# Optimization experiments

Measured on AMD Instinct MI355X. Metric: run time of the kernel, lower is better.

The kernel has to match this reference:

```python
import jax, jax.numpy as jnp
import numpy as np

NUM_QUERIES = 300


def setup_inputs() -> dict:
    key = jax.random.key(0)
    k1, k2, k3 = jax.random.split(key, 3)
    d_model = 256
    tokens = jax.random.normal(k1, (16, 20000, d_model), dtype=jnp.float32)
    # nn.Linear(d_model, 1): weight [1, d_model], bias [1]; store as vector/scalar
    W = jax.random.normal(k2, (d_model,), dtype=jnp.float32) / np.sqrt(d_model)
    b = jax.random.normal(k3, (), dtype=jnp.float32) * 0.01
    return {"tokens": tokens, "W": W, "b": b}


def reference(tokens, W, b):
    # scores: [B, N] -- scalar linear projection per token
    scores = jnp.einsum("bnd,d->bn", tokens, W) + b
    k = min(NUM_QUERIES, tokens.shape[1])
    _, topk = jax.lax.top_k(scores, k)  # [B, k], sorted by descending score
    # gather full token vectors at selected indices: [B, k, d]
    selected = jnp.take_along_axis(tokens, topk[..., None], axis=1)
    return selected, topk
```

## Files before the change

### kernel.cpp

```cpp
#include <hip/hip_runtime.h>
#include <stdint.h>

#define B 16
#define N 20000
#define D 256
#define K 300

__global__ __launch_bounds__(256) void score_kernel(
    const float* __restrict__ tokens, const float* __restrict__ W,
    const float* __restrict__ bias, uint32_t* __restrict__ keys) {
  int gwave = (blockIdx.x * blockDim.x + threadIdx.x) >> 6;
  int lane = threadIdx.x & 63;
  if (gwave >= B * N) return;
  const float4 w4 = ((const float4*)W)[lane];
  const float4 t4 = ((const float4*)(tokens + (size_t)gwave * D))[lane];
  float dot = t4.x * w4.x + t4.y * w4.y + t4.z * w4.z + t4.w * w4.w;
#pragma unroll
  for (int off = 32; off >= 1; off >>= 1) dot += __shfl_xor(dot, off, 64);
  if (lane == 0) {
    float s = dot + bias[0];
    uint32_t u = __float_as_uint(s);
    keys[gwave] = (u & 0x80000000u) ? ~u : (u | 0x80000000u);
  }
}

__global__ __launch_bounds__(1024) void topk_kernel(
    const uint32_t* __restrict__ keys_g, int* __restrict__ idx_out,
    float* __restrict__ out_idx_f) {
  __shared__ uint32_t hist[256];
  __shared__ uint32_t s_prefix, s_remaining, cand_cnt;
  __shared__ uint64_t cand[512];

  const int b = blockIdx.x;
  const int t = threadIdx.x;
  const uint32_t* keys = keys_g + (size_t)b * N;

  if (t == 0) {
    s_prefix = 0;
    s_remaining = K;
    cand_cnt = 0;
  }
  __syncthreads();

  for (int pass = 0; pass < 4; ++pass) {
    int shift = 24 - pass * 8;
    if (t < 256) hist[t] = 0;
    __syncthreads();
    uint32_t prefix = s_prefix;
    uint32_t pmask = (pass == 0) ? 0u : (0xFFFFFFFFu << (shift + 8));
    for (int i = t; i < N; i += 1024) {
      uint32_t k = keys[i];
      if ((k & pmask) == prefix) atomicAdd(&hist[(k >> shift) & 0xFFu], 1u);
    }
    __syncthreads();
    if (t == 0) {
      uint32_t rem = s_remaining;
      uint32_t acc = 0;
      int bin = 255;
      for (; bin > 0; --bin) {
        if (acc + hist[bin] >= rem) break;
        acc += hist[bin];
      }
      s_prefix = prefix | ((uint32_t)bin << shift);
      s_remaining = rem - acc;
    }
    __syncthreads();
  }
  const uint32_t T = s_prefix;

  for (int i = t; i < N; i += 1024) {
    uint32_t k = keys[i];
    if (k >= T) {
      uint32_t pos = atomicAdd(&cand_cnt, 1u);
      if (pos < 512)
        cand[pos] = ((uint64_t)k << 32) | (uint64_t)(0xFFFFFFFFu - (uint32_t)i);
    }
  }
  __syncthreads();
  int cnt = (int)cand_cnt;
  if (cnt > 512) cnt = 512;
  if (t < 512 && t >= cnt) cand[t] = 0;
  __syncthreads();

  for (int ksz = 2; ksz <= 512; ksz <<= 1) {
    for (int j = ksz >> 1; j >= 1; j >>= 1) {
      if (t < 512) {
        int ixj = t ^ j;
        if (ixj > t) {
          uint64_t a = cand[t], c = cand[ixj];
          bool desc = ((t & ksz) == 0);
          if (desc ? (a < c) : (a > c)) {
            cand[t] = c;
            cand[ixj] = a;
          }
        }
      }
      __syncthreads();
    }
  }

  if (t < K) {
    int idx = (int)(0xFFFFFFFFu - (uint32_t)(cand[t] & 0xFFFFFFFFu));
    idx_out[b * K + t] = idx;
    out_idx_f[b * K + t] = (float)idx;
  }
}

__global__ __launch_bounds__(256) void gather_kernel(
    const float* __restrict__ tokens, const int* __restrict__ idx,
    float* __restrict__ out0) {
  int gwave = (blockIdx.x * blockDim.x + threadIdx.x) >> 6;
  int lane = threadIdx.x & 63;
  if (gwave >= B * K) return;
  int b = gwave / K;
  int id = idx[gwave];
  float4 v = ((const float4*)(tokens + ((size_t)b * N + id) * D))[lane];
  ((float4*)(out0 + (size_t)gwave * D))[lane] = v;
}

extern "C" void kernel_launch(void* const* d_in, const int* in_sizes, int n_in,
                              void* d_out, int out_size, void* d_ws,
                              size_t ws_size, hipStream_t stream) {
  const float* tokens = (const float*)d_in[0];
  const float* W = (const float*)d_in[1];
  const float* bias = (const float*)d_in[2];

  float* out_sel = (float*)d_out;
  float* out_idx_f = out_sel + (size_t)B * K * D;

  uint32_t* keys = (uint32_t*)d_ws;
  int* idx = (int*)((char*)d_ws + (size_t)B * N * sizeof(uint32_t));

  score_kernel<<<(B * N + 3) / 4, 256, 0, stream>>>(tokens, W, bias, keys);
  topk_kernel<<<B, 1024, 0, stream>>>(keys, idx, out_idx_f);
  gather_kernel<<<(B * K + 3) / 4, 256, 0, stream>>>(tokens, idx, out_sel);
}
```

Before: 479.4 us.

## Score four tokens per wave and parallelize top-k histogram scan

The score kernel now has each wave process four consecutive tokens, issuing four independent float4 loads and interleaved shuffle reductions, and storing the four keys with a single uint4 write. The top-k kernel reads keys as uint4, and replaces the serial single-thread bin scan with a 64-lane wave prefix scan to pick the threshold bin. It also clears the histogram at the end of each pass, which removes one barrier per pass. The goal is more memory-level parallelism in the bandwidth-bound scoring pass and less serial latency in the radix select, at the cost of more registers and a launch grid that assumes B*N is divisible by 16.

```diff
diff --git a/kernel.cpp b/kernel.cpp
--- a/kernel.cpp
+++ b/kernel.cpp
@@ -9,72 +9,119 @@
 __global__ __launch_bounds__(256) void score_kernel(
     const float* __restrict__ tokens, const float* __restrict__ W,
     const float* __restrict__ bias, uint32_t* __restrict__ keys) {
-  int gwave = (blockIdx.x * blockDim.x + threadIdx.x) >> 6;
+  int wid = (blockIdx.x * blockDim.x + threadIdx.x) >> 6;
   int lane = threadIdx.x & 63;
-  if (gwave >= B * N) return;
+  int tb = wid * 4;
+  if (tb >= B * N) return;
   const float4 w4 = ((const float4*)W)[lane];
-  const float4 t4 = ((const float4*)(tokens + (size_t)gwave * D))[lane];
-  float dot = t4.x * w4.x + t4.y * w4.y + t4.z * w4.z + t4.w * w4.w;
+  const float4* tp = (const float4*)(tokens + (size_t)tb * D);
+  float4 a0 = tp[lane];
+  float4 a1 = tp[64 + lane];
+  float4 a2 = tp[128 + lane];
+  float4 a3 = tp[192 + lane];
+  float d0 = a0.x * w4.x + a0.y * w4.y + a0.z * w4.z + a0.w * w4.w;
+  float d1 = a1.x * w4.x + a1.y * w4.y + a1.z * w4.z + a1.w * w4.w;
+  float d2 = a2.x * w4.x + a2.y * w4.y + a2.z * w4.z + a2.w * w4.w;
+  float d3 = a3.x * w4.x + a3.y * w4.y + a3.z * w4.z + a3.w * w4.w;
 #pragma unroll
-  for (int off = 32; off >= 1; off >>= 1) dot += __shfl_xor(dot, off, 64);
+  for (int off = 32; off >= 1; off >>= 1) {
+    d0 += __shfl_xor(d0, off, 64);
+    d1 += __shfl_xor(d1, off, 64);
+    d2 += __shfl_xor(d2, off, 64);
+    d3 += __shfl_xor(d3, off, 64);
+  }
   if (lane == 0) {
-    float s = dot + bias[0];
-    uint32_t u = __float_as_uint(s);
-    keys[gwave] = (u & 0x80000000u) ? ~u : (u | 0x80000000u);
+    float bb = bias[0];
+    float s0 = d0 + bb, s1 = d1 + bb, s2 = d2 + bb, s3 = d3 + bb;
+    uint32_t u0 = __float_as_uint(s0), u1 = __float_as_uint(s1);
+    uint32_t u2 = __float_as_uint(s2), u3 = __float_as_uint(s3);
+    uint4 kv;
+    kv.x = (u0 & 0x80000000u) ? ~u0 : (u0 | 0x80000000u);
+    kv.y = (u1 & 0x80000000u) ? ~u1 : (u1 | 0x80000000u);
+    kv.z = (u2 & 0x80000000u) ? ~u2 : (u2 | 0x80000000u);
+    kv.w = (u3 & 0x80000000u) ? ~u3 : (u3 | 0x80000000u);
+    ((uint4*)keys)[wid] = kv;
   }
 }
 
 __global__ __launch_bounds__(1024) void topk_kernel(
     const uint32_t* __restrict__ keys_g, int* __restrict__ idx_out,
     float* __restrict__ out_idx_f) {
-  __shared__ uint32_t hist[256];
-  __shared__ uint32_t s_prefix, s_remaining, cand_cnt;
+  __shared__ __align__(16) uint32_t hist[256];
   __shared__ uint64_t cand[512];
+  __shared__ uint32_t s_prefix, s_remaining, s_prefix_next, s_rem_next,
+      cand_cnt;
 
   const int b = blockIdx.x;
   const int t = threadIdx.x;
-  const uint32_t* keys = keys_g + (size_t)b * N;
+  const uint4* keys4 = (const uint4*)(keys_g + (size_t)b * N);
+  const int N4 = N / 4;
 
   if (t == 0) {
     s_prefix = 0;
     s_remaining = K;
     cand_cnt = 0;
   }
+  if (t < 256) hist[t] = 0;
   __syncthreads();
 
   for (int pass = 0; pass < 4; ++pass) {
-    int shift = 24 - pass * 8;
-    if (t < 256) hist[t] = 0;
+    const int shift = 24 - pass * 8;
+    const uint32_t prefix = s_prefix;
+    const uint32_t pmask = (pass == 0) ? 0u : (0xFFFFFFFFu << (shift + 8));
+    for (int i = t; i < N4; i += 1024) {
+      uint4 kv = keys4[i];
+      uint32_t ka[4] = {kv.x, kv.y, kv.z, kv.w};
+#pragma unroll
+      for (int j = 0; j < 4; ++j)
+        if ((ka[j] & pmask) == prefix)
+          atomicAdd(&hist[(ka[j] >> shift) & 255u], 1u);
+    }
     __syncthreads();
-    uint32_t prefix = s_prefix;
-    uint32_t pmask = (pass == 0) ? 0u : (0xFFFFFFFFu << (shift + 8));
-    for (int i = t; i < N; i += 1024) {
-      uint32_t k = keys[i];
-      if ((k & pmask) == prefix) atomicAdd(&hist[(k >> shift) & 0xFFu], 1u);
+    if (t < 64) {
+      uint4 h = ((const uint4*)hist)[t];
+      uint32_t hv0 = h.x, hv1 = h.y, hv2 = h.z, hv3 = h.w;
+      uint32_t sum4 = hv0 + hv1 + hv2 + hv3;
+      uint32_t s = sum4;
+#pragma unroll
+      for (int off = 1; off < 64; off <<= 1) {
+        uint32_t v = __shfl_down(s, off, 64);
+        if (t + off < 64) s += v;
+      }
+      uint32_t rem = s_remaining;
+      uint32_t acc = s - sum4;
+      uint32_t hv[4] = {hv0, hv1, hv2, hv3};
+#pragma unroll
+      for (int j = 3; j >= 0; --j) {
+        uint32_t ge = acc + hv[j];
+        if (acc < rem && rem <= ge) {
+          s_prefix_next = prefix | ((uint32_t)(4 * t + j) << shift);
+          s_rem_next = rem - acc;
+        }
+        acc = ge;
+      }
     }
     __syncthreads();
     if (t == 0) {
-      uint32_t rem = s_remaining;
-      uint32_t acc = 0;
-      int bin = 255;
-      for (; bin > 0; --bin) {
-        if (acc + hist[bin] >= rem) break;
-        acc += hist[bin];
-      }
-      s_prefix = prefix | ((uint32_t)bin << shift);
-      s_remaining = rem - acc;
+      s_prefix = s_prefix_next;
+      s_remaining = s_rem_next;
     }
+    if (t < 256) hist[t] = 0;
     __syncthreads();
   }
   const uint32_t T = s_prefix;
 
-  for (int i = t; i < N; i += 1024) {
-    uint32_t k = keys[i];
-    if (k >= T) {
-      uint32_t pos = atomicAdd(&cand_cnt, 1u);
-      if (pos < 512)
-        cand[pos] = ((uint64_t)k << 32) | (uint64_t)(0xFFFFFFFFu - (uint32_t)i);
-    }
+  for (int i = t; i < N4; i += 1024) {
+    uint4 kv = keys4[i];
+    uint32_t ka[4] = {kv.x, kv.y, kv.z, kv.w};
+#pragma unroll
+    for (int j = 0; j < 4; ++j)
+      if (ka[j] >= T) {
+        uint32_t pos = atomicAdd(&cand_cnt, 1u);
+        if (pos < 512)
+          cand[pos] = ((uint64_t)ka[j] << 32) |
+                      (uint64_t)(0xFFFFFFFFu - (uint32_t)(4 * i + j));
+      }
   }
   __syncthreads();
   int cnt = (int)cand_cnt;
@@ -131,7 +178,7 @@
   uint32_t* keys = (uint32_t*)d_ws;
   int* idx = (int*)((char*)d_ws + (size_t)B * N * sizeof(uint32_t));
 
-  score_kernel<<<(B * N + 3) / 4, 256, 0, stream>>>(tokens, W, bias, keys);
+  score_kernel<<<(B * N) / 16, 256, 0, stream>>>(tokens, W, bias, keys);
   topk_kernel<<<B, 1024, 0, stream>>>(keys, idx, out_idx_f);
   gather_kernel<<<(B * K + 3) / 4, 256, 0, stream>>>(tokens, idx, out_sel);
 }
```

Measured after the change: 448.7 us. 1.07x faster.
